# Optimization experiments

Hardware: AMD Instinct MI355X
Metric: run time of the kernel (lower is better)

The kernel has to match this reference:

```python
import jax, jax.numpy as jnp
import numpy as np

BN_EPS = 1e-5


def setup_inputs() -> dict:
    key = jax.random.key(0)
    ks = jax.random.split(key, 10)
    d = {}
    # EEG-style input: [B, 1, T, electrodes]
    d["x"] = jax.random.normal(ks[0], (512, 1, 1125, 5), dtype=jnp.float32)
    # conv_time: Conv2d(1, 40, (25, 1)) with bias
    d["conv_time_w"] = jax.random.normal(ks[1], (40, 1, 25, 1), dtype=jnp.float32) * 0.05
    d["conv_time_b"] = jax.random.normal(ks[2], (40,), dtype=jnp.float32) * 0.05
    # conv_spat: Conv2d(40, 40, (1, 5), bias=False)
    d["conv_spat_w"] = jax.random.normal(ks[3], (40, 40, 1, 5), dtype=jnp.float32) * 0.05
    # BatchNorm2d(40), eval mode (running stats)
    d["bn_gamma"] = jnp.ones((40,), jnp.float32)
    d["bn_beta"] = jnp.zeros((40,), jnp.float32)
    d["bn_mean"] = jnp.zeros((40,), jnp.float32)
    d["bn_var"] = jnp.ones((40,), jnp.float32)
    # LSTM(input=40, hidden=10): torch layout W_ih [4H, in], W_hh [4H, H]
    d["w_ih"] = jax.random.normal(ks[4], (40, 40), dtype=jnp.float32) * 0.1
    d["w_hh"] = jax.random.normal(ks[5], (40, 10), dtype=jnp.float32) * 0.1
    d["b_ih"] = jax.random.normal(ks[6], (40,), dtype=jnp.float32) * 0.1
    d["b_hh"] = jax.random.normal(ks[7], (40,), dtype=jnp.float32) * 0.1
    # classifier: Linear(10, 2)
    d["fc_w"] = jax.random.normal(ks[8], (2, 10), dtype=jnp.float32) * 0.1
    d["fc_b"] = jnp.zeros((2,), jnp.float32)
    return d


def reference(x, conv_time_w, conv_time_b, conv_spat_w,
              bn_gamma, bn_beta, bn_mean, bn_var,
              w_ih, w_hh, b_ih, b_hh, fc_w, fc_b):
    dn = ("NCHW", "OIHW", "NCHW")
    # conv over time: [B,1,T,5] -> [B,40,T-24,5]
    h = jax.lax.conv_general_dilated(x, conv_time_w, (1, 1), "VALID", dimension_numbers=dn)
    h = h + conv_time_b[None, :, None, None]
    # conv over electrodes: [B,40,T-24,5] -> [B,40,T-24,1]
    h = jax.lax.conv_general_dilated(h, conv_spat_w, (1, 1), "VALID", dimension_numbers=dn)
    # BatchNorm2d (eval, running stats)
    scale = bn_gamma / jnp.sqrt(bn_var + BN_EPS)
    h = h * scale[None, :, None, None] + (bn_beta - bn_mean * scale)[None, :, None, None]
    # AvgPool2d kernel (25,1) stride (5,1): -> [B,40,L,1], L = (T-24-25)//5 + 1
    h = jax.lax.reduce_window(h, 0.0, jax.lax.add, (1, 1, 25, 1), (1, 1, 5, 1), "VALID") / 25.0
    # Dropout2d in eval mode = identity
    # squeeze width + transpose(1,2): [B,40,L] -> [B,L,40]
    h = jnp.transpose(h[..., 0], (0, 2, 1))
    B = h.shape[0]
    H = w_hh.shape[1]  # hidden = 10
    # precompute input-to-gate projection for all timesteps: [L, B, 4H]
    xg = jnp.einsum("blf,gf->lbg", h, w_ih) + b_ih + b_hh

    def step(carry, xt):
        h_prev, c_prev = carry
        gates = xt + h_prev @ w_hh.T          # [B, 4H]
        i, f, g, o = jnp.split(gates, 4, axis=-1)
        i = jax.nn.sigmoid(i)
        f = jax.nn.sigmoid(f)
        g = jnp.tanh(g)
        o = jax.nn.sigmoid(o)
        c = f * c_prev + i * g
        hn = o * jnp.tanh(c)
        return (hn, c), None

    init = (jnp.zeros((B, H), h.dtype), jnp.zeros((B, H), h.dtype))
    (h_last, _), _ = jax.lax.scan(step, init, xg)  # return_seq=False -> last hidden
    return h_last @ fc_w.T + fc_b  # [B, 2]
```

## Files before the change

### kernel.cpp

```cpp
#include <hip/hip_runtime.h>

#define LOG2E 1.44269504088896340736f

typedef float v2f __attribute__((ext_vector_type(2)));
typedef float v4f __attribute__((ext_vector_type(4)));

__device__ __forceinline__ float bf2f(unsigned short u) {
    union { unsigned u32; float f; } v; v.u32 = ((unsigned)u) << 16; return v.f;
}
__device__ __forceinline__ unsigned short f2bf(float f) {
    union { float f; unsigned u32; } v; v.f = f;
    unsigned r = (v.u32 + 0x7FFFu + ((v.u32 >> 16) & 1u)) >> 16;
    return (unsigned short)r;
}
__device__ __forceinline__ bool probe_bf16(const void* gma) {
    return *(const unsigned int*)gma == 0x3F803F80u;
}
__device__ __forceinline__ float ldmix(const void* p, int i, bool bf) {
    return bf ? bf2f(((const unsigned short*)p)[i]) : ((const float*)p)[i];
}
__device__ __forceinline__ float dpp_shl(float x, const int n) {
    int r;
    if (n == 1)      r = __builtin_amdgcn_update_dpp(0, __float_as_int(x), 0x101, 0xF, 0xF, true);
    else if (n == 2) r = __builtin_amdgcn_update_dpp(0, __float_as_int(x), 0x102, 0xF, 0xF, true);
    else             r = __builtin_amdgcn_update_dpp(0, __float_as_int(x), 0x103, 0xF, 0xF, true);
    return __int_as_float(r);
}
#if __has_builtin(__builtin_amdgcn_exp2f)
__device__ __forceinline__ float fexp2(float x) { return __builtin_amdgcn_exp2f(x); }
#else
__device__ __forceinline__ float fexp2(float x) {
    float r; asm("v_exp_f32 %0, %1" : "=v"(r) : "v"(x)); return r;
}
#endif

__global__ __launch_bounds__(1024) void prep_kernel(
    const void* __restrict__ ctw,
    const void* __restrict__ ctb,
    const void* __restrict__ csw,
    const void* __restrict__ gma,
    const void* __restrict__ bta,
    const void* __restrict__ mea,
    const void* __restrict__ var,
    const void* __restrict__ wih,
    const void* __restrict__ bih,
    const void* __restrict__ bhh,
    float* __restrict__ Wg,
    float* __restrict__ Bg)
{
    __shared__ float s_wt[1000];
    __shared__ float s_bt[40];
    __shared__ float s_sp[8000];
    __shared__ float s_wih[1600];
    __shared__ float s_scale[40], s_shift[40];
    __shared__ float s_Wc[5000];
    __shared__ float s_P[5200];
    __shared__ float s_Bc[40];
    __shared__ float s_Wp[9920];

    const int t = threadIdx.x;
    const bool bf = probe_bf16(gma);

    for (int i = t; i < 1000; i += 1024) s_wt[i] = ldmix(ctw, i, bf);
    for (int i = t; i < 8000; i += 1024) s_sp[i] = ldmix(csw, i, bf);
    for (int i = t; i < 1600; i += 1024) s_wih[i] = ldmix(wih, i, bf);
    if (t < 40) {
        s_bt[t] = ldmix(ctb, t, bf);
        float sc = ldmix(gma, t, bf) * rsqrtf(ldmix(var, t, bf) + 1e-5f);
        s_scale[t] = sc;
        s_shift[t] = ldmix(bta, t, bf) - ldmix(mea, t, bf) * sc;
    }
    __syncthreads();

    if (t < 200) {
        const int oc = t / 5, kq = (t % 5) * 5;
        float acc[5][5];
        #pragma unroll
        for (int q = 0; q < 5; ++q)
            #pragma unroll
            for (int e = 0; e < 5; ++e) acc[q][e] = 0.f;
        for (int ic = 0; ic < 40; ++ic) {
            float wtv[5], spv[5];
            #pragma unroll
            for (int q = 0; q < 5; ++q) wtv[q] = s_wt[ic * 25 + kq + q];
            #pragma unroll
            for (int e = 0; e < 5; ++e) spv[e] = s_sp[(oc * 40 + ic) * 5 + e];
            #pragma unroll
            for (int q = 0; q < 5; ++q)
                #pragma unroll
                for (int e = 0; e < 5; ++e) acc[q][e] = fmaf(wtv[q], spv[e], acc[q][e]);
        }
        const float sc = s_scale[oc];
        #pragma unroll
        for (int q = 0; q < 5; ++q)
            #pragma unroll
            for (int e = 0; e < 5; ++e)
                s_Wc[(oc * 25 + kq + q) * 5 + e] = acc[q][e] * sc;
    }
    if (t >= 512 && t < 552) {
        const int oc = t - 512;
        float a = 0.f;
        for (int ic = 0; ic < 40; ++ic) {
            float se = 0.f;
            #pragma unroll
            for (int e = 0; e < 5; ++e) se += s_sp[(oc * 40 + ic) * 5 + e];
            a = fmaf(se, s_bt[ic], a);
        }
        s_Bc[oc] = a * s_scale[oc] + s_shift[oc];
    }
    __syncthreads();

    if (t < 200) {
        const int oc = t / 5, e = t % 5;
        float run = 0.f;
        s_P[oc * 130 + e] = 0.f;
        for (int k = 0; k < 25; ++k) {
            run += s_Wc[(oc * 25 + k) * 5 + e];
            s_P[oc * 130 + (k + 1) * 5 + e] = run;
        }
    }
    __syncthreads();

    for (int i = t; i < 9800; i += 1024) {
        const int oc = i / 245, rem = i % 245, j = rem / 5, e = rem % 5;
        const int lo = j - 24 > 0 ? j - 24 : 0;
        const int hi = j < 24 ? j : 24;
        float val = (s_P[oc * 130 + (hi + 1) * 5 + e] - s_P[oc * 130 + lo * 5 + e]) * 0.04f;
        s_Wp[oc * 248 + rem] = val;
    }
    if (t < 120) s_Wp[(t / 3) * 248 + 245 + (t % 3)] = 0.f;
    __syncthreads();

    if (t < 620) {
        const int gp = t / 31, ko = t % 31;
        const int g0 = 2 * gp, kf0 = 8 * ko;
        float acc0[8], acc1[8];
        #pragma unroll
        for (int q = 0; q < 8; ++q) { acc0[q] = 0.f; acc1[q] = 0.f; }
        for (int oc = 0; oc < 40; ++oc) {
            const float4 pa = *reinterpret_cast<const float4*>(&s_Wp[oc * 248 + kf0]);
            const float4 pb = *reinterpret_cast<const float4*>(&s_Wp[oc * 248 + kf0 + 4]);
            const float wa = s_wih[g0 * 40 + oc];
            const float wb = s_wih[(g0 + 1) * 40 + oc];
            acc0[0] = fmaf(wa, pa.x, acc0[0]); acc0[1] = fmaf(wa, pa.y, acc0[1]);
            acc0[2] = fmaf(wa, pa.z, acc0[2]); acc0[3] = fmaf(wa, pa.w, acc0[3]);
            acc0[4] = fmaf(wa, pb.x, acc0[4]); acc0[5] = fmaf(wa, pb.y, acc0[5]);
            acc0[6] = fmaf(wa, pb.z, acc0[6]); acc0[7] = fmaf(wa, pb.w, acc0[7]);
            acc1[0] = fmaf(wb, pa.x, acc1[0]); acc1[1] = fmaf(wb, pa.y, acc1[1]);
            acc1[2] = fmaf(wb, pa.z, acc1[2]); acc1[3] = fmaf(wb, pa.w, acc1[3]);
            acc1[4] = fmaf(wb, pb.x, acc1[4]); acc1[5] = fmaf(wb, pb.y, acc1[5]);
            acc1[6] = fmaf(wb, pb.z, acc1[6]); acc1[7] = fmaf(wb, pb.w, acc1[7]);
        }
        #pragma unroll
        for (int q = 0; q < 8; ++q) {
            Wg[g0 * 248 + kf0 + q]       = acc0[q];
            Wg[(g0 + 1) * 248 + kf0 + q] = acc1[q];
        }
    }
    if (t >= 640 && t < 680) {
        const int g = t - 640;
        float a = ldmix(bih, g, bf) + ldmix(bhh, g, bf);
        for (int oc = 0; oc < 40; ++oc) a = fmaf(s_wih[g * 40 + oc], s_Bc[oc], a);
        Bg[g] = a;
    }
}

__global__ __launch_bounds__(256) void conv_kernel(
    const void* __restrict__ x,
    const float* __restrict__ Wg,
    const float* __restrict__ Bg,
    const void* __restrict__ gma,
    float* __restrict__ xg)
{
    __shared__ float sw[9920];
    __shared__ float u[8856];

    const int b   = blockIdx.x;
    const int tid = threadIdx.x;
    const bool bf = probe_bf16(gma);

    {
        const float4* wsrc = reinterpret_cast<const float4*>(Wg);
        float4* wdst = reinterpret_cast<float4*>(sw);
        for (int i = tid; i < 2480; i += 256) wdst[i] = wsrc[i];
    }
    if (bf) {
        const unsigned short* xp = (const unsigned short*)x + b * 5625;
        for (int i = tid; i < 5625; i += 256) u[i] = bf2f(xp[i]);
    } else {
        const float* xp = (const float*)x + b * 5625;
        for (int i = tid; i < 5625; i += 256) u[i] = xp[i];
    }
    for (int i = 5625 + tid; i < 6144; i += 256) u[i] = 0.f;
    __syncthreads();

    const int wave = __builtin_amdgcn_readfirstlane(tid >> 6);
    const int lane = tid & 63;
    const int gb   = 10 * wave;
    const int a0 = 25 * lane;
    const int a1 = 25 * (lane + 54);
    const int a2 = 25 * (lane + 108);
    const int a3 = 25 * (lane + 162);

    v4f acc[10];
    #pragma unroll
    for (int gi = 0; gi < 10; ++gi) {
        float bgv = Bg[gb + gi];
        acc[gi] = (v4f){bgv, bgv, bgv, bgv};
    }

    const int wrow = gb * 248;
    for (int k = 0; k < 248; k += 4) {
        v4f xv0 = (v4f){ u[a0 + k],     u[a1 + k],     u[a2 + k],     u[a3 + k]     };
        v4f xv1 = (v4f){ u[a0 + k + 1], u[a1 + k + 1], u[a2 + k + 1], u[a3 + k + 1] };
        v4f xv2 = (v4f){ u[a0 + k + 2], u[a1 + k + 2], u[a2 + k + 2], u[a3 + k + 2] };
        v4f xv3 = (v4f){ u[a0 + k + 3], u[a1 + k + 3], u[a2 + k + 3], u[a3 + k + 3] };
        #pragma unroll
        for (int gi = 0; gi < 10; ++gi) {
            const float4 w = *reinterpret_cast<const float4*>(&sw[wrow + gi * 248 + k]);
            acc[gi] += xv0 * w.x;
            acc[gi] += xv1 * w.y;
            acc[gi] += xv2 * w.z;
            acc[gi] += xv3 * w.w;
        }
    }
    __syncthreads();

    const float km = (wave == 2) ? 2.0f * LOG2E : -LOG2E;
    if (lane < 54) {
        #pragma unroll
        for (int gi = 0; gi < 10; ++gi) {
            const int p = 4 * gi + wave;
            u[lane * 41 + p]         = km * acc[gi].x;
            u[(lane + 54) * 41 + p]  = km * acc[gi].y;
            u[(lane + 108) * 41 + p] = km * acc[gi].z;
            u[(lane + 162) * 41 + p] = km * acc[gi].w;
        }
    }
    __syncthreads();

    float* dst = xg + b * 9280;
    for (int i = tid; i < 9280; i += 256) {
        const int row = i / 40, col = i - 40 * row;
        dst[i] = (row < 216) ? u[row * 41 + col] : 0.f;
    }
}

__global__ __launch_bounds__(256) void lstm_kernel(
    const float* __restrict__ xg,
    const void* __restrict__ whh_p,
    const void* __restrict__ fcw_p,
    const void* __restrict__ fcb_p,
    const void* __restrict__ gma,
    void* __restrict__ out)
{
    const int tid  = threadIdx.x;
    const int wave = __builtin_amdgcn_readfirstlane(tid >> 6);
    const int lane = tid & 63;
    const int b    = blockIdx.x * 4 + wave;
    const bool bf  = probe_bf16(gma);

    const int m  = lane < 40 ? lane : 39;
    const int j  = m >> 2;
    const int t  = m & 3;
    const int gl = 10 * t + j;

    const float L2   = 2.0f * LOG2E;
    const float kmul = (t == 2) ?  L2 : -LOG2E;
    const float aact = (t == 2) ? -2.0f : (t == 0 ? L2 : 1.0f);
    const float bact = (t == 2) ?  1.0f : 0.0f;

    float whhr[10];
    #pragma unroll
    for (int mm = 0; mm < 10; ++mm) whhr[mm] = kmul * ldmix(whh_p, gl * 10 + mm, bf);

    const float* xp = xg + b * 9280 + m;
    float xb[12];
    #pragma unroll
    for (int p = 0; p < 12; ++p) xb[p] = xp[p * 40];

    float cs = 0.f, h = 0.f;

    for (int l = 0; l < 216; l += 12) {
        #pragma unroll
        for (int s = 0; s < 12; ++s) {
            float xv = xb[s];
            xb[s] = xp[(l + s + 12) * 40];
            float h0 = __int_as_float(__builtin_amdgcn_readlane(__float_as_int(h), 0));
            float h1 = __int_as_float(__builtin_amdgcn_readlane(__float_as_int(h), 4));
            float h2 = __int_as_float(__builtin_amdgcn_readlane(__float_as_int(h), 8));
            float h3 = __int_as_float(__builtin_amdgcn_readlane(__float_as_int(h), 12));
            float h4 = __int_as_float(__builtin_amdgcn_readlane(__float_as_int(h), 16));
            float h5 = __int_as_float(__builtin_amdgcn_readlane(__float_as_int(h), 20));
            float h6 = __int_as_float(__builtin_amdgcn_readlane(__float_as_int(h), 24));
            float h7 = __int_as_float(__builtin_amdgcn_readlane(__float_as_int(h), 28));
            float h8 = __int_as_float(__builtin_amdgcn_readlane(__float_as_int(h), 32));
            float h9 = __int_as_float(__builtin_amdgcn_readlane(__float_as_int(h), 36));
            float a_ = fmaf(whhr[0], h0, xv);
            a_ = fmaf(whhr[1], h1, a_);
            a_ = fmaf(whhr[2], h2, a_);
            float b_ = whhr[3] * h3;
            b_ = fmaf(whhr[4], h4, b_);
            b_ = fmaf(whhr[5], h5, b_);
            float c_ = whhr[6] * h6;
            c_ = fmaf(whhr[7], h7, c_);
            float d_ = whhr[8] * h8;
            d_ = fmaf(whhr[9], h9, d_);
            float accg = (a_ + b_) + (c_ + d_);
            float tt  = fexp2(accg);
            float rr  = __builtin_amdgcn_rcpf(1.0f + tt);
            float act = fmaf(aact, rr, bact);
            float fv = dpp_shl(act, 1);
            float gv = dpp_shl(act, 2);
            float ov = dpp_shl(act, 3);
            cs = fmaf(fv, cs, act * gv);
            float t2 = fexp2(cs);
            float r2 = __builtin_amdgcn_rcpf(1.0f + t2);
            float th = fmaf(-2.0f, r2, 1.0f);
            h = ov * th;
        }
    }

    float w0[10], w1[10];
    #pragma unroll
    for (int mm = 0; mm < 10; ++mm) {
        w0[mm] = ldmix(fcw_p, mm, bf);
        w1[mm] = ldmix(fcw_p, 10 + mm, bf);
    }
    float o0 = ldmix(fcb_p, 0, bf), o1 = ldmix(fcb_p, 1, bf);
    #pragma unroll
    for (int mm = 0; mm < 10; ++mm) {
        float hm = __int_as_float(__builtin_amdgcn_readlane(__float_as_int(h), 4 * mm));
        o0 = fmaf(w0[mm], hm, o0);
        o1 = fmaf(w1[mm], hm, o1);
    }
    if (lane == 0) {
        if (bf) {
            ((unsigned short*)out)[b * 2]     = f2bf(o0);
            ((unsigned short*)out)[b * 2 + 1] = f2bf(o1);
        } else {
            ((float*)out)[b * 2]     = o0;
            ((float*)out)[b * 2 + 1] = o1;
        }
    }
}

__global__ __launch_bounds__(256, 2) void fused_kernel(
    const void* __restrict__ x,
    const float* __restrict__ Wg,
    const float* __restrict__ Bg,
    const void* __restrict__ whh_p,
    const void* __restrict__ fcw_p,
    const void* __restrict__ fcb_p,
    const void* __restrict__ gma,
    void* __restrict__ out)
{
    __shared__ float sw[9920];
    __shared__ float u[8960];

    const int b   = blockIdx.x;
    const int tid = threadIdx.x;
    const bool bf = probe_bf16(gma);

    for (int i = tid; i < 9920; i += 256) sw[i] = Wg[i];
    if (bf) {
        const unsigned short* xp = (const unsigned short*)x + b * 5625;
        for (int i = tid; i < 5625; i += 256) u[i] = bf2f(xp[i]);
    } else {
        const float* xp = (const float*)x + b * 5625;
        for (int i = tid; i < 5625; i += 256) u[i] = xp[i];
    }
    for (int i = 5625 + tid; i < 6144; i += 256) u[i] = 0.f;
    for (int i = 8640 + tid; i < 8960; i += 256) u[i] = 0.f;
    __syncthreads();

    const int wave  = __builtin_amdgcn_readfirstlane(tid >> 6);
    const int lane  = tid & 63;
    const int gb    = 20 * (wave & 1);
    const int lbase = 108 * (wave >> 1);
    const int l0 = lbase + lane;
    const int l1 = l0 + 64;
    const int a0 = 25 * l0, a1 = 25 * l1;

    v2f acc[20];
    #pragma unroll
    for (int gi = 0; gi < 20; ++gi) {
        float bgv = Bg[gb + gi];
        acc[gi] = (v2f){bgv, bgv};
    }

    const int wrow = gb * 248;
    for (int k = 0; k < 248; k += 4) {
        v2f xv0 = (v2f){ u[a0 + k],     u[a1 + k]     };
        v2f xv1 = (v2f){ u[a0 + k + 1], u[a1 + k + 1] };
        v2f xv2 = (v2f){ u[a0 + k + 2], u[a1 + k + 2] };
        v2f xv3 = (v2f){ u[a0 + k + 3], u[a1 + k + 3] };
        #pragma unroll
        for (int gi = 0; gi < 20; ++gi) {
            const float4 w = *reinterpret_cast<const float4*>(&sw[wrow + gi * 248 + k]);
            acc[gi] += xv0 * w.x;
            acc[gi] += xv1 * w.y;
            acc[gi] += xv2 * w.z;
            acc[gi] += xv3 * w.w;
        }
    }
    __syncthreads();

    #pragma unroll
    for (int gi = 0; gi < 20; ++gi) {
        u[l0 * 40 + gb + gi] = acc[gi].x;
        if (lane < 44) u[l1 * 40 + gb + gi] = acc[gi].y;
    }
    __syncthreads();

    if (wave != 0) return;

    const int j   = lane >> 2;
    const int jt  = lane & 3;
    const int jj  = j < 10 ? j : 9;
    const int gl  = 10 * jt + jj;

    const float L2   = 2.0f * LOG2E;
    const float kmul = (jt == 2) ?  L2 : -LOG2E;
    const float aact = (jt == 2) ? -2.0f : (jt == 0 ? L2 : 1.0f);
    const float bact = (jt == 2) ?  1.0f : 0.0f;

    float whhr[10];
    #pragma unroll
    for (int m = 0; m < 10; ++m) whhr[m] = kmul * ldmix(whh_p, gl * 10 + m, bf);

    float xb[6];
    #pragma unroll
    for (int p = 0; p < 6; ++p) xb[p] = kmul * u[p * 40 + gl];

    float cs = 0.f, h = 0.f;

    for (int l = 0; l < 216; l += 6) {
        #pragma unroll
        for (int s = 0; s < 6; ++s) {
            float xv = xb[s];
            xb[s] = kmul * u[(l + s + 6) * 40 + gl];
            float a_ = xv, b_ = 0.f;
            #pragma unroll
            for (int m = 0; m < 10; m += 2) {
                float h0 = __int_as_float(__builtin_amdgcn_readlane(__float_as_int(h), 4 * m));
                float h1 = __int_as_float(__builtin_amdgcn_readlane(__float_as_int(h), 4 * (m + 1)));
                a_ = fmaf(whhr[m], h0, a_);
                b_ = fmaf(whhr[m + 1], h1, b_);
            }
            float accg = a_ + b_;
            float tt  = fexp2(accg);
            float rr  = __builtin_amdgcn_rcpf(1.0f + tt);
            float act = fmaf(aact, rr, bact);
            float fv = dpp_shl(act, 1);
            float gv = dpp_shl(act, 2);
            float ov = dpp_shl(act, 3);
            cs = fmaf(fv, cs, act * gv);
            float t2 = fexp2(cs);
            float r2 = __builtin_amdgcn_rcpf(1.0f + t2);
            float th = fmaf(-2.0f, r2, 1.0f);
            h = ov * th;
        }
    }

    float w0[10], w1[10];
    #pragma unroll
    for (int m = 0; m < 10; ++m) {
        w0[m] = ldmix(fcw_p, m, bf);
        w1[m] = ldmix(fcw_p, 10 + m, bf);
    }
    float o0 = ldmix(fcb_p, 0, bf), o1 = ldmix(fcb_p, 1, bf);
    #pragma unroll
    for (int m = 0; m < 10; ++m) {
        float hm = __int_as_float(__builtin_amdgcn_readlane(__float_as_int(h), 4 * m));
        o0 = fmaf(w0[m], hm, o0);
        o1 = fmaf(w1[m], hm, o1);
    }
    if (lane == 0) {
        if (bf) {
            ((unsigned short*)out)[b * 2]     = f2bf(o0);
            ((unsigned short*)out)[b * 2 + 1] = f2bf(o1);
        } else {
            ((float*)out)[b * 2]     = o0;
            ((float*)out)[b * 2 + 1] = o1;
        }
    }
}

extern "C" void kernel_launch(void* const* d_in, const int* in_sizes, int n_in,
                              void* d_out, int out_size, void* d_ws, size_t ws_size,
                              hipStream_t stream) {
    const void* x    = d_in[0];
    const void* ctw  = d_in[1];
    const void* ctb  = d_in[2];
    const void* csw  = d_in[3];
    const void* gma  = d_in[4];
    const void* bta  = d_in[5];
    const void* mea  = d_in[6];
    const void* var  = d_in[7];
    const void* wih  = d_in[8];
    const void* whh  = d_in[9];
    const void* bih  = d_in[10];
    const void* bhh  = d_in[11];
    const void* fcw  = d_in[12];
    const void* fcb  = d_in[13];

    char* ws = (char*)d_ws;
    float* Wg = (float*)ws;
    float* Bg = (float*)(ws + 40 * 248 * 4);
    float* xg = (float*)(ws + 40960);

    const size_t need = 40960u + 512u * 232u * 40u * 4u;

    prep_kernel<<<1, 1024, 0, stream>>>(ctw, ctb, csw, gma, bta, mea, var,
                                        wih, bih, bhh, Wg, Bg);
    if (ws_size >= need) {
        conv_kernel<<<512, 256, 0, stream>>>(x, Wg, Bg, gma, xg);
        lstm_kernel<<<128, 256, 0, stream>>>(xg, whh, fcw, fcb, gma, d_out);
    } else {
        fused_kernel<<<512, 256, 0, stream>>>(x, Wg, Bg, whh, fcw, fcb, gma, d_out);
    }
}
```

Before: 170.6 us.

## Run fused conv projection on MFMA with split-bf16 three-pass emulation

Replaces the scalar FP32 FMA loop in conv_kernel with bf16 MFMA 16x16x32 instructions. Near-FP32 accuracy is kept by splitting inputs and weights into high and low bf16 parts and summing three products. A new prep2 kernel packs the weights into per-lane MFMA fragment layout in workspace. The input tile is stored in LDS as paired bf16 values, including shifted copies so odd-offset rows stay aligned. The gate outputs are written straight to global memory without the LDS transpose, at the cost of an extra launch, more workspace and a small precision loss.

Result: slower. 194.6 us (+14.0%).

```diff
diff --git a/kernel.cpp b/kernel.cpp
--- a/kernel.cpp
+++ b/kernel.cpp
@@ -3,7 +3,8 @@
 #define LOG2E 1.44269504088896340736f
 
 typedef float v2f __attribute__((ext_vector_type(2)));
-typedef float v4f __attribute__((ext_vector_type(4)));
+typedef short bf16x8 __attribute__((ext_vector_type(8)));
+typedef float f32x4 __attribute__((ext_vector_type(4)));
 
 __device__ __forceinline__ float bf2f(unsigned short u) {
     union { unsigned u32; float f; } v; v.u32 = ((unsigned)u) << 16; return v.f;
@@ -35,18 +36,12 @@
 #endif
 
 __global__ __launch_bounds__(1024) void prep_kernel(
-    const void* __restrict__ ctw,
-    const void* __restrict__ ctb,
-    const void* __restrict__ csw,
-    const void* __restrict__ gma,
-    const void* __restrict__ bta,
-    const void* __restrict__ mea,
-    const void* __restrict__ var,
-    const void* __restrict__ wih,
-    const void* __restrict__ bih,
-    const void* __restrict__ bhh,
-    float* __restrict__ Wg,
-    float* __restrict__ Bg)
+    const void* __restrict__ ctw, const void* __restrict__ ctb,
+    const void* __restrict__ csw, const void* __restrict__ gma,
+    const void* __restrict__ bta, const void* __restrict__ mea,
+    const void* __restrict__ var, const void* __restrict__ wih,
+    const void* __restrict__ bih, const void* __restrict__ bhh,
+    float* __restrict__ Wg, float* __restrict__ Bg)
 {
     __shared__ float s_wt[1000];
     __shared__ float s_bt[40];
@@ -165,84 +160,133 @@
     }
 }
 
+__global__ __launch_bounds__(256) void prep2_kernel(
+    const float* __restrict__ Wg, unsigned* __restrict__ wfrag)
+{
+    const int D = blockIdx.x * 256 + threadIdx.x;
+    const int dw = D & 3, lane = (D >> 2) & 63, rest = D >> 8;
+    const int nt = rest % 3, rr = rest / 3, kst = rr & 7, plane = rr >> 3;
+    const int n  = nt * 16 + (lane & 15);
+    const int k0 = kst * 32 + ((lane >> 4) << 3) + 2 * dw;
+    float v0 = (n < 40 && k0     < 248) ? Wg[n * 248 + k0]     : 0.f;
+    float v1 = (n < 40 && k0 + 1 < 248) ? Wg[n * 248 + k0 + 1] : 0.f;
+    unsigned short e0, e1;
+    if (plane == 0) { e0 = f2bf(v0); e1 = f2bf(v1); }
+    else {
+        e0 = f2bf(v0 - bf2f(f2bf(v0)));
+        e1 = f2bf(v1 - bf2f(f2bf(v1)));
+    }
+    wfrag[D] = (unsigned)e0 | ((unsigned)e1 << 16);
+}
+
 __global__ __launch_bounds__(256) void conv_kernel(
     const void* __restrict__ x,
-    const float* __restrict__ Wg,
     const float* __restrict__ Bg,
+    const unsigned* __restrict__ wfrag,
     const void* __restrict__ gma,
     float* __restrict__ xg)
 {
-    __shared__ float sw[9920];
-    __shared__ float u[8856];
+    __shared__ unsigned xp[11776];
 
     const int b   = blockIdx.x;
     const int tid = threadIdx.x;
     const bool bf = probe_bf16(gma);
 
-    {
-        const float4* wsrc = reinterpret_cast<const float4*>(Wg);
-        float4* wdst = reinterpret_cast<float4*>(sw);
-        for (int i = tid; i < 2480; i += 256) wdst[i] = wsrc[i];
-    }
-    if (bf) {
-        const unsigned short* xp = (const unsigned short*)x + b * 5625;
-        for (int i = tid; i < 5625; i += 256) u[i] = bf2f(xp[i]);
-    } else {
-        const float* xp = (const float*)x + b * 5625;
-        for (int i = tid; i < 5625; i += 256) u[i] = xp[i];
-    }
-    for (int i = 5625 + tid; i < 6144; i += 256) u[i] = 0.f;
+    for (int i = 0; i < 12; ++i) {
+        const int d = tid + 256 * i;
+        if (d < 2944) {
+            const int e = 2 * d;
+            float x0 = 0.f, x1 = 0.f, x2 = 0.f;
+            if (bf) {
+                const unsigned short* q = (const unsigned short*)x + b * 5625;
+                if (e     < 5625) x0 = bf2f(q[e]);
+                if (e + 1 < 5625) x1 = bf2f(q[e + 1]);
+                if (e + 2 < 5625) x2 = bf2f(q[e + 2]);
+            } else {
+                const float* q = (const float*)x + b * 5625;
+                if (e     < 5625) x0 = q[e];
+                if (e + 1 < 5625) x1 = q[e + 1];
+                if (e + 2 < 5625) x2 = q[e + 2];
+            }
+            const unsigned short h0 = f2bf(x0), h1 = f2bf(x1), h2 = f2bf(x2);
+            const unsigned short l0 = f2bf(x0 - bf2f(h0));
+            const unsigned short l1 = f2bf(x1 - bf2f(h1));
+            const unsigned short l2 = f2bf(x2 - bf2f(h2));
+            xp[d]        = (unsigned)h0 | ((unsigned)h1 << 16);
+            xp[2944 + d] = (unsigned)h1 | ((unsigned)h2 << 16);
+            xp[5888 + d] = (unsigned)l0 | ((unsigned)l1 << 16);
+            xp[8832 + d] = (unsigned)l1 | ((unsigned)l2 << 16);
+        }
+    }
     __syncthreads();
 
     const int wave = __builtin_amdgcn_readfirstlane(tid >> 6);
     const int lane = tid & 63;
-    const int gb   = 10 * wave;
-    const int a0 = 25 * lane;
-    const int a1 = 25 * (lane + 54);
-    const int a2 = 25 * (lane + 108);
-    const int a3 = 25 * (lane + 162);
-
-    v4f acc[10];
-    #pragma unroll
-    for (int gi = 0; gi < 10; ++gi) {
-        float bgv = Bg[gb + gi];
-        acc[gi] = (v4f){bgv, bgv, bgv, bgv};
-    }
-
-    const int wrow = gb * 248;
-    for (int k = 0; k < 248; k += 4) {
-        v4f xv0 = (v4f){ u[a0 + k],     u[a1 + k],     u[a2 + k],     u[a3 + k]     };
-        v4f xv1 = (v4f){ u[a0 + k + 1], u[a1 + k + 1], u[a2 + k + 1], u[a3 + k + 1] };
-        v4f xv2 = (v4f){ u[a0 + k + 2], u[a1 + k + 2], u[a2 + k + 2], u[a3 + k + 2] };
-        v4f xv3 = (v4f){ u[a0 + k + 3], u[a1 + k + 3], u[a2 + k + 3], u[a3 + k + 3] };
-        #pragma unroll
-        for (int gi = 0; gi < 10; ++gi) {
-            const float4 w = *reinterpret_cast<const float4*>(&sw[wrow + gi * 248 + k]);
-            acc[gi] += xv0 * w.x;
-            acc[gi] += xv1 * w.y;
-            acc[gi] += xv2 * w.z;
-            acc[gi] += xv3 * w.w;
-        }
-    }
-    __syncthreads();
-
-    const float km = (wave == 2) ? 2.0f * LOG2E : -LOG2E;
-    if (lane < 54) {
-        #pragma unroll
-        for (int gi = 0; gi < 10; ++gi) {
-            const int p = 4 * gi + wave;
-            u[lane * 41 + p]         = km * acc[gi].x;
-            u[(lane + 54) * 41 + p]  = km * acc[gi].y;
-            u[(lane + 108) * 41 + p] = km * acc[gi].z;
-            u[(lane + 162) * 41 + p] = km * acc[gi].w;
-        }
-    }
-    __syncthreads();
+    const int col  = lane & 15;
+    const int quad = lane >> 4;
+    const int mstart = (wave < 2) ? 4 * wave : (wave == 2 ? 8 : 11);
+    const int mcount = (wave < 2) ? 4 : 3;
+
+    const int pbase = (col & 1) ? 2944 : 0;
+    const int laneA = ((25 * col - (col & 1)) >> 1) + quad * 4;
+
+    f32x4 acc[4][3];
+    #pragma unroll
+    for (int mt = 0; mt < 4; ++mt)
+        #pragma unroll
+        for (int nt = 0; nt < 3; ++nt) acc[mt][nt] = (f32x4){0.f, 0.f, 0.f, 0.f};
+
+    union AF { unsigned u[4]; bf16x8 v; };
+
+    for (int kst = 0; kst < 8; ++kst) {
+        AF Bh[3], Bl[3];
+        #pragma unroll
+        for (int nt = 0; nt < 3; ++nt) {
+            const uint4 bh = *reinterpret_cast<const uint4*>(
+                wfrag + (((kst) * 3 + nt) * 64 + lane) * 4);
+            const uint4 bl = *reinterpret_cast<const uint4*>(
+                wfrag + (((8 + kst) * 3 + nt) * 64 + lane) * 4);
+            Bh[nt].u[0] = bh.x; Bh[nt].u[1] = bh.y; Bh[nt].u[2] = bh.z; Bh[nt].u[3] = bh.w;
+            Bl[nt].u[0] = bl.x; Bl[nt].u[1] = bl.y; Bl[nt].u[2] = bl.z; Bl[nt].u[3] = bl.w;
+        }
+        for (int mt = 0; mt < mcount; ++mt) {
+            const int db = pbase + laneA + kst * 16 + 200 * (mstart + mt);
+            AF Ah, Al;
+            Ah.u[0] = xp[db];     Ah.u[1] = xp[db + 1];
+            Ah.u[2] = xp[db + 2]; Ah.u[3] = xp[db + 3];
+            Al.u[0] = xp[5888 + db];     Al.u[1] = xp[5888 + db + 1];
+            Al.u[2] = xp[5888 + db + 2]; Al.u[3] = xp[5888 + db + 3];
+            #pragma unroll
+            for (int nt = 0; nt < 3; ++nt)
+                acc[mt][nt] = __builtin_amdgcn_mfma_f32_16x16x32_bf16(
+                    Ah.v, Bh[nt].v, acc[mt][nt], 0, 0, 0);
+            #pragma unroll
+            for (int nt = 0; nt < 3; ++nt)
+                acc[mt][nt] = __builtin_amdgcn_mfma_f32_16x16x32_bf16(
+                    Ah.v, Bl[nt].v, acc[mt][nt], 0, 0, 0);
+            #pragma unroll
+            for (int nt = 0; nt < 3; ++nt)
+                acc[mt][nt] = __builtin_amdgcn_mfma_f32_16x16x32_bf16(
+                    Al.v, Bh[nt].v, acc[mt][nt], 0, 0, 0);
+        }
+    }
 
     float* dst = xg + b * 9280;
-    for (int i = tid; i < 9280; i += 256) {
-        const int row = i / 40, col = i - 40 * row;
-        dst[i] = (row < 216) ? u[row * 41 + col] : 0.f;
+    #pragma unroll
+    for (int nt = 0; nt < 3; ++nt) {
+        const int g = nt * 16 + col;
+        if (g < 40) {
+            const int ty = g / 10, q = g - 10 * ty;
+            const int p  = 4 * q + ty;
+            const float km = (ty == 2) ? 2.0f * LOG2E : -LOG2E;
+            const float bg = Bg[g];
+            for (int mt = 0; mt < mcount; ++mt) {
+                const int r0 = (mstart + mt) * 16 + quad * 4;
+                #pragma unroll
+                for (int r = 0; r < 4; ++r)
+                    dst[(r0 + r) * 40 + p] = (acc[mt][nt][r] + bg) * km;
+            }
+        }
     }
 }
 
@@ -364,11 +408,11 @@
 
     for (int i = tid; i < 9920; i += 256) sw[i] = Wg[i];
     if (bf) {
-        const unsigned short* xp = (const unsigned short*)x + b * 5625;
-        for (int i = tid; i < 5625; i += 256) u[i] = bf2f(xp[i]);
+        const unsigned short* xq = (const unsigned short*)x + b * 5625;
+        for (int i = tid; i < 5625; i += 256) u[i] = bf2f(xq[i]);
     } else {
-        const float* xp = (const float*)x + b * 5625;
-        for (int i = tid; i < 5625; i += 256) u[i] = xp[i];
+        const float* xq = (const float*)x + b * 5625;
+        for (int i = tid; i < 5625; i += 256) u[i] = xq[i];
     }
     for (int i = 5625 + tid; i < 6144; i += 256) u[i] = 0.f;
     for (int i = 8640 + tid; i < 8960; i += 256) u[i] = 0.f;
@@ -506,16 +550,18 @@
     const void* fcb  = d_in[13];
 
     char* ws = (char*)d_ws;
-    float* Wg = (float*)ws;
-    float* Bg = (float*)(ws + 40 * 248 * 4);
-    float* xg = (float*)(ws + 40960);
-
-    const size_t need = 40960u + 512u * 232u * 40u * 4u;
+    float* Wg       = (float*)ws;
+    float* Bg       = (float*)(ws + 40 * 248 * 4);
+    unsigned* wfrag = (unsigned*)(ws + 40960);
+    float* xg       = (float*)(ws + 40960 + 49152);
+
+    const size_t need = 40960u + 49152u + 512u * 232u * 40u * 4u;
 
     prep_kernel<<<1, 1024, 0, stream>>>(ctw, ctb, csw, gma, bta, mea, var,
                                         wih, bih, bhh, Wg, Bg);
     if (ws_size >= need) {
-        conv_kernel<<<512, 256, 0, stream>>>(x, Wg, Bg, gma, xg);
+        prep2_kernel<<<48, 256, 0, stream>>>(Wg, wfrag);
+        conv_kernel<<<512, 256, 0, stream>>>(x, Bg, wfrag, gma, xg);
         lstm_kernel<<<128, 256, 0, stream>>>(xg, whh, fcw, fcb, gma, d_out);
     } else {
         fused_kernel<<<512, 256, 0, stream>>>(x, Wg, Bg, whh, fcw, fcb, gma, d_out);
```
